# Optimization experiments

Measured on AMD Instinct MI355X. Metric: run time of the kernel, lower is better.

## Reference

```python
import jax, jax.numpy as jnp
import numpy as np

B, T = 4, 8
H, W = 120, 160
NON_SEM = 4
CAT = 16
MAP_CH = NON_SEM + CAT          # 20 map channels
FEAT_CH = 2 * NON_SEM + CAT     # 24 feature channels
RES = 5.0                       # cm per map cell
GLOBAL_M, LOCAL_M = 960, 240    # map_size/resolution, and /downscale
M2 = LOCAL_M * LOCAL_M
HFOV = 79.0
CAM_H_CM = 88.0
VISION_CM = 100 * RES           # vision_range cells -> cm
AGENT_R2 = 2.0 ** 2
EXPLORE_R2 = 3.0 ** 2
FX = W / (2.0 * float(np.tan(np.deg2rad(HFOV) / 2.0)))
FY = FX
CX, CY = W / 2.0, H / 2.0

LOCAL_POSE0 = jnp.array([LOCAL_M * RES / 2, LOCAL_M * RES / 2, 0.0], jnp.float32)
GLOBAL_POSE0 = jnp.array([GLOBAL_M * RES / 2, GLOBAL_M * RES / 2, 0.0], jnp.float32)
OFF = (GLOBAL_M - LOCAL_M) // 2
BOUNDS0 = jnp.array([OFF, OFF + LOCAL_M, OFF, OFF + LOCAL_M], jnp.int32)
ORIGINS0 = jnp.array([OFF * RES, OFF * RES, 0.0], jnp.float32)


def _splat1(flat, w):  # scatter-add scalar weights into the flattened local grid
    return jnp.zeros((M2,), jnp.float32).at[flat].add(w)


def _splatC(flat, vals):  # vals [C, N] -> [C, M2]
    return jnp.zeros((vals.shape[0], M2), jnp.float32).at[:, flat].add(vals)


def _step(carry, xs):
    lmap, gmap, lpose, gpose, bounds, origins = carry
    obs, delta, cam_T, done, upd = xs
    doneb = done != 0
    # per-env reset on episode end (init_map_and_pose_for_env)
    lmap = jnp.where(doneb[:, None, None, None], 0.0, lmap)
    gmap = jnp.where(doneb[:, None, None, None], 0.0, gmap)
    lpose = jnp.where(doneb[:, None], LOCAL_POSE0, lpose)
    gpose = jnp.where(doneb[:, None], GLOBAL_POSE0, gpose)
    bounds = jnp.where(doneb[:, None], BOUNDS0, bounds)
    origins = jnp.where(doneb[:, None], ORIGINS0, origins)

    # dead-reckoning pose update (delta in agent frame)
    th = jnp.deg2rad(lpose[:, 2])
    dx = delta[:, 0] * jnp.cos(th) - delta[:, 1] * jnp.sin(th)
    dy = delta[:, 0] * jnp.sin(th) + delta[:, 1] * jnp.cos(th)
    lpose = lpose + jnp.stack([dx, dy, delta[:, 2]], -1)

    # depth -> camera-frame point cloud (cm)
    depth = obs[:, 3] * 400.0 + 50.0  # [B,H,W]
    sem = obs[:, NON_SEM:]            # [B,CAT,H,W]
    uu = (jnp.arange(W, dtype=jnp.float32) - CX)[None, None, :]
    vv = (CY - jnp.arange(H, dtype=jnp.float32))[None, :, None]
    pts = jnp.stack([uu * depth / FX, vv * depth / FY, depth, jnp.ones_like(depth)], -1)
    pts = jnp.einsum('bij,bhwj->bhwi', cam_T, pts)  # camera extrinsics
    x_f, y_l, z_u = pts[..., 2], -pts[..., 0], pts[..., 1] + CAM_H_CM

    # agent frame -> local map frame
    th2 = jnp.deg2rad(lpose[:, 2])[:, None, None]
    wx = lpose[:, 0][:, None, None] + x_f * jnp.cos(th2) - y_l * jnp.sin(th2)
    wy = lpose[:, 1][:, None, None] + x_f * jnp.sin(th2) + y_l * jnp.cos(th2)
    ix = jnp.floor(wx / RES).astype(jnp.int32)
    iy = jnp.floor(wy / RES).astype(jnp.int32)
    valid = (depth > 25.0) & (depth < VISION_CM) & (ix >= 0) & (ix < LOCAL_M) & (iy >= 0) & (iy < LOCAL_M)
    flat = (jnp.clip(iy, 0, LOCAL_M - 1) * LOCAL_M + jnp.clip(ix, 0, LOCAL_M - 1)).reshape(B, -1)
    vm = valid.reshape(B, -1).astype(jnp.float32)
    obst_w = vm * ((z_u > 25.0) & (z_u < 150.0)).reshape(B, -1).astype(jnp.float32)

    exp_grid = jax.vmap(_splat1)(flat, vm).reshape(B, LOCAL_M, LOCAL_M)
    obst_grid = jax.vmap(_splat1)(flat, obst_w).reshape(B, LOCAL_M, LOCAL_M)
    sem_grid = jax.vmap(_splatC)(flat, sem.reshape(B, CAT, -1) * vm[:, None, :]).reshape(B, CAT, LOCAL_M, LOCAL_M)

    # agent location / been-close disks
    g = jnp.arange(LOCAL_M, dtype=jnp.float32)
    dxg = g[None, None, :] - (lpose[:, 0] / RES)[:, None, None]
    dyg = g[None, :, None] - (lpose[:, 1] / RES)[:, None, None]
    d2 = dxg * dxg + dyg * dyg
    agent = (d2 <= AGENT_R2).astype(jnp.float32)
    close = (d2 <= EXPLORE_R2).astype(jnp.float32)

    lmap = jnp.concatenate([
        jnp.maximum(lmap[:, 0], jnp.clip(obst_grid, 0.0, 1.0))[:, None],
        jnp.maximum(lmap[:, 1], jnp.clip(exp_grid, 0.0, 1.0))[:, None],
        agent[:, None],
        jnp.maximum(lmap[:, 3], close)[:, None],
        jnp.maximum(lmap[:, NON_SEM:], jnp.clip(sem_grid, 0.0, 1.0)),
    ], axis=1)

    # fuse local window into global map for envs flagged for update
    y1, x1 = bounds[:, 0], bounds[:, 2]
    crop = jax.vmap(lambda gm, y, x: jax.lax.dynamic_slice(gm, (0, y, x), (MAP_CH, LOCAL_M, LOCAL_M)))(gmap, y1, x1)
    updb = (upd != 0)[:, None, None, None]
    fused = jnp.where(updb, jnp.maximum(crop, lmap), crop)
    gmap = jax.vmap(lambda gm, c, y, x: jax.lax.dynamic_update_slice(gm, c, (0, y, x)))(gmap, fused, y1, x1)
    gpose = jnp.where((upd != 0)[:, None], lpose + origins, gpose)

    feats = jnp.concatenate([lmap[:, :NON_SEM], fused[:, :NON_SEM], lmap[:, NON_SEM:]], axis=1)
    return (lmap, gmap, lpose, gpose, bounds, origins), (feats, lpose, gpose, bounds, origins)


def _forward(obs_seq, pose_delta, cam_poses, init_local_map, init_global_map,
             init_local_pose, init_global_pose, init_origins,
             done_flags, update_flags, init_bounds):
    xs = (obs_seq.swapaxes(0, 1), pose_delta.swapaxes(0, 1), cam_poses.swapaxes(0, 1),
          done_flags.swapaxes(0, 1), update_flags.swapaxes(0, 1))
    carry0 = (init_local_map, init_global_map, init_local_pose, init_global_pose, init_bounds, init_origins)
    carry, ys = jax.lax.scan(_step, carry0, xs)
    feats, lp, gp, bnds, orgs = ys
    return (feats.swapaxes(0, 1), carry[0], carry[1], lp.swapaxes(0, 1), gp.swapaxes(0, 1),
            bnds.swapaxes(0, 1), orgs.swapaxes(0, 1))


def setup_inputs() -> dict:
    key = jax.random.key(0)
    ks = jax.random.split(key, 5)
    obs_seq = jax.random.uniform(ks[0], (B, T, MAP_CH, H, W), jnp.float32)
    pose_delta = jax.random.normal(ks[1], (B, T, 3), jnp.float32) * jnp.array([10.0, 2.0, 5.0], jnp.float32)
    cam_poses = jnp.eye(4, dtype=jnp.float32)[None, None] + 0.02 * jax.random.normal(ks[2], (B, T, 4, 4), jnp.float32)
    done_flags = jax.random.randint(ks[3], (B, T), 0, 2, jnp.int32)
    update_flags = jax.random.randint(ks[4], (B, T), 0, 2, jnp.int32)
    return {
        'obs_seq': obs_seq,
        'pose_delta': pose_delta,
        'done_flags': done_flags,
        'update_flags': update_flags,
        'cam_poses': cam_poses,
        'init_local_map': jnp.zeros((B, MAP_CH, LOCAL_M, LOCAL_M), jnp.float32),
        'init_global_map': jnp.zeros((B, MAP_CH, GLOBAL_M, GLOBAL_M), jnp.float32),
        'init_local_pose': jnp.tile(LOCAL_POSE0[None], (B, 1)),
        'init_global_pose': jnp.tile(GLOBAL_POSE0[None], (B, 1)),
        'init_bounds': jnp.tile(BOUNDS0[None], (B, 1)),
        'init_origins': jnp.tile(ORIGINS0[None], (B, 1)),
    }


def reference(obs_seq, pose_delta, done_flags, update_flags, cam_poses,
              init_local_map, init_global_map, init_local_pose, init_global_pose,
              init_bounds, init_origins):
    return _forward(obs_seq, pose_delta, cam_poses, init_local_map, init_global_map,
                    init_local_pose, init_global_pose, init_origins,
                    done_flags, update_flags, init_bounds)
```

## Files before the change

kernel.cpp:

```cpp
#include <hip/hip_runtime.h>
#include <math.h>

#define Bn 4
#define Tn 8
#define Hn 120
#define Wn 160
#define HWn (Hn * Wn)
#define NON_SEMn 4
#define CATn 16
#define MAP_CHn 20
#define FEAT_CHn 24
#define LOCAL_Mn 240
#define GLOBAL_Mn 960
#define M2n (LOCAL_Mn * LOCAL_Mn)
#define TBMn (Tn * Bn * M2n)
#define Pn (Tn * Bn * HWn)
#define NBLK_SCAN 1800
#define UPD_BLKS ((Bn * M2n + 255) / 256)
#define GMAP_BLKS ((Bn * MAP_CHn * GLOBAL_Mn * GLOBAL_Mn / 4 + 255) / 256)

#define DEG2RADf ((float)0.017453292519943295)

typedef float vf4 __attribute__((ext_vector_type(4)));

#define OUT_FEATS 0
#define OUT_LMAP  44236800
#define OUT_GMAP  48844800
#define OUT_LP    122572800
#define OUT_GP    122572896
#define OUT_BNDS  122572992
#define OUT_ORGS  122573120

#define WS_LPOSE  0
#define WS_ANYD   96
#define WS_REC2   128
#define WS_BSUM   (WS_REC2 + 2 * TBMn)
#define WS_CELL   (WS_BSUM + 2048)
#define WS_RECB   (WS_CELL + Pn)


__global__ void pose_kernel(const float* __restrict__ pose_delta,
                            const int* __restrict__ done_flags,
                            const int* __restrict__ upd_flags,
                            const float* __restrict__ init_lpose,
                            const float* __restrict__ init_gpose,
                            const int* __restrict__ init_bounds,
                            const float* __restrict__ init_origins,
                            float* __restrict__ ws_lpose,
                            float* __restrict__ ws_anydone,
                            float* __restrict__ out_lp,
                            float* __restrict__ out_gp,
                            float* __restrict__ out_bnds,
                            float* __restrict__ out_orgs) {
#pragma clang fp contract(off)
    int b = threadIdx.x;
    if (b >= Bn) return;
    float lx = init_lpose[b * 3 + 0], ly = init_lpose[b * 3 + 1], lz = init_lpose[b * 3 + 2];
    float gx = init_gpose[b * 3 + 0], gy = init_gpose[b * 3 + 1], gz = init_gpose[b * 3 + 2];
    int b0 = init_bounds[b * 4 + 0], b1 = init_bounds[b * 4 + 1];
    int b2i = init_bounds[b * 4 + 2], b3 = init_bounds[b * 4 + 3];
    float ox = init_origins[b * 3 + 0], oy = init_origins[b * 3 + 1], oz = init_origins[b * 3 + 2];
    float anyd = 0.0f;
    for (int t = 0; t < Tn; t++) {
        int done = done_flags[b * Tn + t];
        int upd  = upd_flags[b * Tn + t];
        if (done) {
            lx = 600.0f; ly = 600.0f; lz = 0.0f;
            gx = 2400.0f; gy = 2400.0f; gz = 0.0f;
            b0 = 360; b1 = 600; b2i = 360; b3 = 600;
            ox = 1800.0f; oy = 1800.0f; oz = 0.0f;
            anyd = 1.0f;
        }
        float th = lz * DEG2RADf;
        float c = cosf(th), s = sinf(th);
        float d0 = pose_delta[(b * Tn + t) * 3 + 0];
        float d1 = pose_delta[(b * Tn + t) * 3 + 1];
        float d2 = pose_delta[(b * Tn + t) * 3 + 2];
        lx = lx + (d0 * c - d1 * s);
        ly = ly + (d0 * s + d1 * c);
        lz = lz + d2;
        if (upd) { gx = lx + ox; gy = ly + oy; gz = lz + oz; }
        ws_lpose[(t * Bn + b) * 3 + 0] = lx;
        ws_lpose[(t * Bn + b) * 3 + 1] = ly;
        ws_lpose[(t * Bn + b) * 3 + 2] = lz;
        out_lp[(b * Tn + t) * 3 + 0] = lx;
        out_lp[(b * Tn + t) * 3 + 1] = ly;
        out_lp[(b * Tn + t) * 3 + 2] = lz;
        out_gp[(b * Tn + t) * 3 + 0] = gx;
        out_gp[(b * Tn + t) * 3 + 1] = gy;
        out_gp[(b * Tn + t) * 3 + 2] = gz;
        out_bnds[(b * Tn + t) * 4 + 0] = (float)b0;
        out_bnds[(b * Tn + t) * 4 + 1] = (float)b1;
        out_bnds[(b * Tn + t) * 4 + 2] = (float)b2i;
        out_bnds[(b * Tn + t) * 4 + 3] = (float)b3;
        out_orgs[(b * Tn + t) * 3 + 0] = ox;
        out_orgs[(b * Tn + t) * 3 + 1] = oy;
        out_orgs[(b * Tn + t) * 3 + 2] = oz;
    }
    ws_anydone[b] = anyd;
}

__global__ void project_kernel(const float* __restrict__ obs,
                               const float* __restrict__ cam,
                               const float* __restrict__ ws_lpose,
                               uint2* __restrict__ rec2,
                               int* __restrict__ cellid,
                               float fx) {
#pragma clang fp contract(off)
    int g = blockIdx.x * blockDim.x + threadIdx.x;
    if (g >= Pn) return;
    int p = g % HWn;
    int tb = g / HWn;
    int b = tb % Bn;
    int t = tb / Bn;
    int h = p / Wn, w = p % Wn;
    const float* ob = obs + (size_t)((b * Tn + t) * MAP_CHn) * HWn;
    float depth = ob[3 * HWn + p] * 400.0f + 50.0f;
    float u = (float)w - 80.0f;
    float v = 60.0f - (float)h;
    float px = u * depth / fx;
    float py = v * depth / fx;
    float pz = depth;
    const float* Tm = cam + (size_t)(b * Tn + t) * 16;
    float X = ((Tm[0] * px + Tm[1] * py) + Tm[2] * pz) + Tm[3];
    float Y = ((Tm[4] * px + Tm[5] * py) + Tm[6] * pz) + Tm[7];
    float Z = ((Tm[8] * px + Tm[9] * py) + Tm[10] * pz) + Tm[11];
    float x_f = Z;
    float y_l = -X;
    float z_u = Y + 88.0f;
    float lx = ws_lpose[(t * Bn + b) * 3 + 0];
    float ly = ws_lpose[(t * Bn + b) * 3 + 1];
    float lz = ws_lpose[(t * Bn + b) * 3 + 2];
    float th2 = lz * DEG2RADf;
    float c2 = cosf(th2), s2 = sinf(th2);
    float wx = (lx + x_f * c2) - y_l * s2;
    float wy = (ly + x_f * s2) + y_l * c2;
    int ix = (int)floorf(wx / 5.0f);
    int iy = (int)floorf(wy / 5.0f);
    bool valid = (depth > 25.0f) && (depth < 500.0f) &&
                 (ix >= 0) && (ix < LOCAL_Mn) && (iy >= 0) && (iy < LOCAL_Mn);
    int cell = -1;
    if (valid) {
        cell = (t * Bn + b) * M2n + iy * LOCAL_Mn + ix;
        unsigned addv = 1u + ((z_u > 25.0f && z_u < 150.0f) ? 65536u : 0u);
        atomicAdd(&rec2[cell].x, addv);
    }
    cellid[g] = cell;
}

__global__ void scan1_kernel(uint2* __restrict__ rec2,
                             unsigned* __restrict__ bsum) {
    __shared__ unsigned s[256];
    int tid = threadIdx.x;
    int base = blockIdx.x * 1024 + tid * 4;
    unsigned v0 = rec2[base].x & 0xFFFFu, v1 = rec2[base + 1].x & 0xFFFFu;
    unsigned v2 = rec2[base + 2].x & 0xFFFFu, v3 = rec2[base + 3].x & 0xFFFFu;
    unsigned tsum = v0 + v1 + v2 + v3;
    s[tid] = tsum;
    __syncthreads();
    for (int d = 1; d < 256; d <<= 1) {
        unsigned a = (tid >= d) ? s[tid - d] : 0u;
        __syncthreads();
        s[tid] += a;
        __syncthreads();
    }
    unsigned excl = s[tid] - tsum;
    if (tid == 255) bsum[blockIdx.x] = s[255];
    rec2[base].y     = excl;
    rec2[base + 1].y = excl + v0;
    rec2[base + 2].y = excl + v0 + v1;
    rec2[base + 3].y = excl + v0 + v1 + v2;
}

__global__ void scan2_kernel(unsigned* __restrict__ bsum) {
    __shared__ unsigned s[256];
    int tid = threadIdx.x;
    unsigned run = 0;
    for (int base = 0; base < NBLK_SCAN; base += 256) {
        int i = base + tid;
        unsigned v = (i < NBLK_SCAN) ? bsum[i] : 0u;
        s[tid] = v;
        __syncthreads();
        for (int d = 1; d < 256; d <<= 1) {
            unsigned a = (tid >= d) ? s[tid - d] : 0u;
            __syncthreads();
            s[tid] += a;
            __syncthreads();
        }
        unsigned tot = s[255];
        if (i < NBLK_SCAN) bsum[i] = run + s[tid] - v;
        run += tot;
        __syncthreads();
    }
}

__global__ void scatter_copy_kernel(const float* __restrict__ obs,
                                    const int* __restrict__ cellid,
                                    const unsigned* __restrict__ bsum,
                                    uint2* __restrict__ rec2,
                                    float* __restrict__ recb) {
    int g = blockIdx.x * blockDim.x + threadIdx.x;
    if (g >= Pn) return;
    int c = cellid[g];
    if (c < 0) return;
    int p = g % HWn;
    int tb = g / HWn;
    int b = tb % Bn;
    int t = tb / Bn;
    const float* ob = obs + (size_t)((b * Tn + t) * MAP_CHn) * HWn;
    vf4 r[4];
#pragma unroll
    for (int q = 0; q < 4; q++) {
        r[q].x = ob[(size_t)(NON_SEMn + 4 * q + 0) * HWn + p];
        r[q].y = ob[(size_t)(NON_SEMn + 4 * q + 1) * HWn + p];
        r[q].z = ob[(size_t)(NON_SEMn + 4 * q + 2) * HWn + p];
        r[q].w = ob[(size_t)(NON_SEMn + 4 * q + 3) * HWn + p];
    }
    unsigned pos = bsum[c >> 10] + atomicAdd(&rec2[c].y, 1u);
    vf4* rp = (vf4*)(recb + (size_t)pos * CATn);
#pragma unroll
    for (int q = 0; q < 4; q++)
        __builtin_nontemporal_store(r[q], rp + q);
}

__global__ void __launch_bounds__(256)
mega_kernel(const uint2* __restrict__ rec2,
            const unsigned* __restrict__ bsum,
            const float* __restrict__ recb,
            const int* __restrict__ done_flags,
            const int* __restrict__ upd_flags,
            const float* __restrict__ ws_lpose,
            const float* __restrict__ init_lmap,
            const float* __restrict__ init_gmap,
            const int* __restrict__ init_bounds,
            const float* __restrict__ anydone,
            float* __restrict__ out_feats,
            float* __restrict__ out_lmap,
            float* __restrict__ out_gmap) {
#pragma clang fp contract(off)
    if (blockIdx.x >= UPD_BLKS) {
        size_t i4 = (size_t)(blockIdx.x - UPD_BLKS) * blockDim.x + threadIdx.x;
        const size_t total4 = (size_t)Bn * MAP_CHn * GLOBAL_Mn * GLOBAL_Mn / 4;
        if (i4 >= total4) return;
        size_t f = i4 * 4;
        int gx = (int)(f % GLOBAL_Mn);
        size_t r = f / GLOBAL_Mn;
        int gy = (int)(r % GLOBAL_Mn);
        size_t bc = r / GLOBAL_Mn;
        int b = (int)(bc / MAP_CHn);
        int y1 = init_bounds[b * 4 + 0];
        int x1 = init_bounds[b * 4 + 2];
        if (gy >= y1 && gy < y1 + LOCAL_Mn && gx >= x1 && gx < x1 + LOCAL_Mn) return;
        vf4 v;
        if (anydone[b] != 0.0f) {
            v = (vf4)(0.0f);
        } else {
            v = __builtin_nontemporal_load((const vf4*)(init_gmap + f));
        }
        __builtin_nontemporal_store(v, (vf4*)(out_gmap + f));
        return;
    }

    int idx = blockIdx.x * blockDim.x + threadIdx.x;
    if (idx >= Bn * M2n) return;
    int b = idx / M2n, j = idx % M2n;
    int y = j / LOCAL_Mn, x = j % LOCAL_Mn;
    int y1 = init_bounds[b * 4 + 0];
    int x1 = init_bounds[b * 4 + 2];

    float lm[MAP_CHn], cr[MAP_CHn];
#pragma unroll
    for (int ch = 0; ch < MAP_CHn; ch++)
        lm[ch] = __builtin_nontemporal_load(init_lmap + ((size_t)(b * MAP_CHn + ch)) * M2n + j);
#pragma unroll
    for (int ch = 0; ch < MAP_CHn; ch++)
        cr[ch] = __builtin_nontemporal_load(
            init_gmap + ((size_t)(b * MAP_CHn + ch) * GLOBAL_Mn + (y1 + y)) * GLOBAL_Mn + (x1 + x));

    for (int t = 0; t < Tn; t++) {
        int done = done_flags[b * Tn + t];
        int upd  = upd_flags[b * Tn + t];
        if (done) {
#pragma unroll
            for (int ch = 0; ch < MAP_CHn; ch++) { lm[ch] = 0.0f; cr[ch] = 0.0f; }
        }
        float lx = ws_lpose[(t * Bn + b) * 3 + 0];
        float ly = ws_lpose[(t * Bn + b) * 3 + 1];
        float dxg = (float)x - lx / 5.0f;
        float dyg = (float)y - ly / 5.0f;
        float d2 = dxg * dxg + dyg * dyg;
        float agent = (d2 <= 4.0f) ? 1.0f : 0.0f;
        float close = (d2 <= 9.0f) ? 1.0f : 0.0f;

        int cell = (t * Bn + b) * M2n + j;
        uint2 rc = rec2[cell];
        unsigned n = rc.x & 0xFFFFu;
        lm[0] = fmaxf(lm[0], (rc.x >> 16) ? 1.0f : 0.0f);
        lm[1] = fmaxf(lm[1], n ? 1.0f : 0.0f);
        lm[2] = agent;
        lm[3] = fmaxf(lm[3], close);

        if (n) {
            unsigned st = bsum[cell >> 10] + rc.y - n;
            float sem[CATn];
#pragma unroll
            for (int c = 0; c < CATn; c++) sem[c] = 0.0f;
            const vf4* rp = (const vf4*)(recb + (size_t)st * CATn);
            for (unsigned k = 0; k < n; k++) {
                vf4 r0 = rp[0], r1 = rp[1], r2 = rp[2], r3 = rp[3];
                rp += 4;
                sem[0] += r0.x;  sem[1] += r0.y;  sem[2] += r0.z;  sem[3] += r0.w;
                sem[4] += r1.x;  sem[5] += r1.y;  sem[6] += r1.z;  sem[7] += r1.w;
                sem[8] += r2.x;  sem[9] += r2.y;  sem[10] += r2.z; sem[11] += r2.w;
                sem[12] += r3.x; sem[13] += r3.y; sem[14] += r3.z; sem[15] += r3.w;
            }
#pragma unroll
            for (int c = 0; c < CATn; c++)
                lm[NON_SEMn + c] = fmaxf(lm[NON_SEMn + c], fminf(fmaxf(sem[c], 0.0f), 1.0f));
        }
        if (upd) {
#pragma unroll
            for (int ch = 0; ch < MAP_CHn; ch++) cr[ch] = fmaxf(cr[ch], lm[ch]);
        }

        size_t fb = ((size_t)(b * Tn + t) * FEAT_CHn) * M2n + j;
#pragma unroll
        for (int ch = 0; ch < NON_SEMn; ch++)
            __builtin_nontemporal_store(lm[ch], out_feats + fb + (size_t)ch * M2n);
#pragma unroll
        for (int ch = 0; ch < NON_SEMn; ch++)
            __builtin_nontemporal_store(cr[ch], out_feats + fb + (size_t)(NON_SEMn + ch) * M2n);
#pragma unroll
        for (int c = 0; c < CATn; c++)
            __builtin_nontemporal_store(lm[NON_SEMn + c], out_feats + fb + (size_t)(2 * NON_SEMn + c) * M2n);
    }

#pragma unroll
    for (int ch = 0; ch < MAP_CHn; ch++)
        __builtin_nontemporal_store(lm[ch], out_lmap + ((size_t)(b * MAP_CHn + ch)) * M2n + j);
#pragma unroll
    for (int ch = 0; ch < MAP_CHn; ch++)
        __builtin_nontemporal_store(
            cr[ch], out_gmap + ((size_t)(b * MAP_CHn + ch) * GLOBAL_Mn + (y1 + y)) * GLOBAL_Mn + (x1 + x));
}

extern "C" void kernel_launch(void* const* d_in, const int* in_sizes, int n_in,
                              void* d_out, int out_size, void* d_ws, size_t ws_size,
                              hipStream_t stream) {
    const float* obs        = (const float*)d_in[0];
    const float* pose_delta = (const float*)d_in[1];
    const int*   done_flags = (const int*)d_in[2];
    const int*   upd_flags  = (const int*)d_in[3];
    const float* cam_poses  = (const float*)d_in[4];
    const float* init_lmap  = (const float*)d_in[5];
    const float* init_gmap  = (const float*)d_in[6];
    const float* init_lpose = (const float*)d_in[7];
    const float* init_gpose = (const float*)d_in[8];
    const int*   init_bnds  = (const int*)d_in[9];
    const float* init_orgs  = (const float*)d_in[10];

    float* out = (float*)d_out;
    float* ws  = (float*)d_ws;

    float*    ws_lpose = ws + WS_LPOSE;
    float*    ws_anyd  = ws + WS_ANYD;
    uint2*    rec2     = (uint2*)(ws + WS_REC2);
    unsigned* bsum     = (unsigned*)(ws + WS_BSUM);
    int*      cellid   = (int*)(ws + WS_CELL);
    float*    recb     = ws + WS_RECB;

    float fx = (float)(160.0 / (2.0 * tan(79.0 * M_PI / 180.0 / 2.0)));

    pose_kernel<<<1, 64, 0, stream>>>(pose_delta, done_flags, upd_flags,
                                      init_lpose, init_gpose, init_bnds, init_orgs,
                                      ws_lpose, ws_anyd,
                                      out + OUT_LP, out + OUT_GP,
                                      out + OUT_BNDS, out + OUT_ORGS);

    (void)hipMemsetAsync(rec2, 0, (size_t)TBMn * sizeof(uint2), stream);

    project_kernel<<<(Pn + 255) / 256, 256, 0, stream>>>(
        obs, cam_poses, ws_lpose, rec2, cellid, fx);

    scan1_kernel<<<NBLK_SCAN, 256, 0, stream>>>(rec2, bsum);
    scan2_kernel<<<1, 256, 0, stream>>>(bsum);

    scatter_copy_kernel<<<(Pn + 255) / 256, 256, 0, stream>>>(
        obs, cellid, bsum, rec2, recb);

    mega_kernel<<<UPD_BLKS + GMAP_BLKS, 256, 0, stream>>>(
        rec2, bsum, recb, done_flags, upd_flags, ws_lpose,
        init_lmap, init_gmap, init_bnds, ws_anyd,
        out + OUT_FEATS, out + OUT_LMAP, out + OUT_GMAP);
}
```

Measured before the change: 837.4 us.

## Fuse pose and global-map copy into projection; replace scan2 with atomic tile offsets

Drops the separate pose kernel: each projection and update thread recomputes its pose by replaying the dead-reckoning recurrence. The large global-map copy moves from the final update kernel into the projection launch, so that bandwidth-bound copy can overlap the atomic-heavy projection. The single-block scan2 kernel is replaced by an atomicAdd on a counter in scan1 that hands each tile a base offset. This works because tiles only need disjoint contiguous segments, not ordered ones. The change removes two launches and serial work at the cost of redundant per-thread trigonometry and unordered tile placement in the record buffer.

New measurement: 842.9 us. About the same (+0.7%).

```diff
diff --git a/kernel.cpp b/kernel.cpp
--- a/kernel.cpp
+++ b/kernel.cpp
@@ -15,8 +15,9 @@
 #define M2n (LOCAL_Mn * LOCAL_Mn)
 #define TBMn (Tn * Bn * M2n)
 #define Pn (Tn * Bn * HWn)
-#define NBLK_SCAN 1800
+#define NTILE_SCAN 1800
 #define UPD_BLKS ((Bn * M2n + 255) / 256)
+#define PROJ_BLKS ((Pn + 255) / 256)
 #define GMAP_BLKS ((Bn * MAP_CHn * GLOBAL_Mn * GLOBAL_Mn / 4 + 255) / 256)
 
 #define DEG2RADf ((float)0.017453292519943295)
@@ -31,46 +32,23 @@
 #define OUT_BNDS  122572992
 #define OUT_ORGS  122573120
 
-#define WS_LPOSE  0
-#define WS_ANYD   96
+#define WS_CNTR   96
 #define WS_REC2   128
 #define WS_BSUM   (WS_REC2 + 2 * TBMn)
 #define WS_CELL   (WS_BSUM + 2048)
 #define WS_RECB   (WS_CELL + Pn)
 
-
-__global__ void pose_kernel(const float* __restrict__ pose_delta,
-                            const int* __restrict__ done_flags,
-                            const int* __restrict__ upd_flags,
-                            const float* __restrict__ init_lpose,
-                            const float* __restrict__ init_gpose,
-                            const int* __restrict__ init_bounds,
-                            const float* __restrict__ init_origins,
-                            float* __restrict__ ws_lpose,
-                            float* __restrict__ ws_anydone,
-                            float* __restrict__ out_lp,
-                            float* __restrict__ out_gp,
-                            float* __restrict__ out_bnds,
-                            float* __restrict__ out_orgs) {
+__device__ __forceinline__ void pose_upto(const float* __restrict__ pose_delta,
+                                          const int* __restrict__ done_flags,
+                                          const float* __restrict__ init_lpose,
+                                          int b, int tt,
+                                          float& lx, float& ly, float& lz) {
 #pragma clang fp contract(off)
-    int b = threadIdx.x;
-    if (b >= Bn) return;
-    float lx = init_lpose[b * 3 + 0], ly = init_lpose[b * 3 + 1], lz = init_lpose[b * 3 + 2];
-    float gx = init_gpose[b * 3 + 0], gy = init_gpose[b * 3 + 1], gz = init_gpose[b * 3 + 2];
-    int b0 = init_bounds[b * 4 + 0], b1 = init_bounds[b * 4 + 1];
-    int b2i = init_bounds[b * 4 + 2], b3 = init_bounds[b * 4 + 3];
-    float ox = init_origins[b * 3 + 0], oy = init_origins[b * 3 + 1], oz = init_origins[b * 3 + 2];
-    float anyd = 0.0f;
-    for (int t = 0; t < Tn; t++) {
-        int done = done_flags[b * Tn + t];
-        int upd  = upd_flags[b * Tn + t];
-        if (done) {
-            lx = 600.0f; ly = 600.0f; lz = 0.0f;
-            gx = 2400.0f; gy = 2400.0f; gz = 0.0f;
-            b0 = 360; b1 = 600; b2i = 360; b3 = 600;
-            ox = 1800.0f; oy = 1800.0f; oz = 0.0f;
-            anyd = 1.0f;
-        }
+    lx = init_lpose[b * 3 + 0];
+    ly = init_lpose[b * 3 + 1];
+    lz = init_lpose[b * 3 + 2];
+    for (int t = 0; t <= tt; t++) {
+        if (done_flags[b * Tn + t]) { lx = 600.0f; ly = 600.0f; lz = 0.0f; }
         float th = lz * DEG2RADf;
         float c = cosf(th), s = sinf(th);
         float d0 = pose_delta[(b * Tn + t) * 3 + 0];
@@ -79,35 +57,96 @@
         lx = lx + (d0 * c - d1 * s);
         ly = ly + (d0 * s + d1 * c);
         lz = lz + d2;
-        if (upd) { gx = lx + ox; gy = ly + oy; gz = lz + oz; }
-        ws_lpose[(t * Bn + b) * 3 + 0] = lx;
-        ws_lpose[(t * Bn + b) * 3 + 1] = ly;
-        ws_lpose[(t * Bn + b) * 3 + 2] = lz;
-        out_lp[(b * Tn + t) * 3 + 0] = lx;
-        out_lp[(b * Tn + t) * 3 + 1] = ly;
-        out_lp[(b * Tn + t) * 3 + 2] = lz;
-        out_gp[(b * Tn + t) * 3 + 0] = gx;
-        out_gp[(b * Tn + t) * 3 + 1] = gy;
-        out_gp[(b * Tn + t) * 3 + 2] = gz;
-        out_bnds[(b * Tn + t) * 4 + 0] = (float)b0;
-        out_bnds[(b * Tn + t) * 4 + 1] = (float)b1;
-        out_bnds[(b * Tn + t) * 4 + 2] = (float)b2i;
-        out_bnds[(b * Tn + t) * 4 + 3] = (float)b3;
-        out_orgs[(b * Tn + t) * 3 + 0] = ox;
-        out_orgs[(b * Tn + t) * 3 + 1] = oy;
-        out_orgs[(b * Tn + t) * 3 + 2] = oz;
-    }
-    ws_anydone[b] = anyd;
-}
-
-__global__ void project_kernel(const float* __restrict__ obs,
-                               const float* __restrict__ cam,
-                               const float* __restrict__ ws_lpose,
-                               uint2* __restrict__ rec2,
-                               int* __restrict__ cellid,
-                               float fx) {
+    }
+}
+
+__global__ void __launch_bounds__(256)
+proj_gmap_kernel(const float* __restrict__ obs,
+                 const float* __restrict__ cam,
+                 const float* __restrict__ pose_delta,
+                 const int* __restrict__ done_flags,
+                 const int* __restrict__ upd_flags,
+                 const float* __restrict__ init_lpose,
+                 const float* __restrict__ init_gpose,
+                 const int* __restrict__ init_bounds,
+                 const float* __restrict__ init_origins,
+                 const float* __restrict__ init_gmap,
+                 uint2* __restrict__ rec2,
+                 int* __restrict__ cellid,
+                 float* __restrict__ out_lp,
+                 float* __restrict__ out_gp,
+                 float* __restrict__ out_bnds,
+                 float* __restrict__ out_orgs,
+                 float* __restrict__ out_gmap,
+                 float fx) {
 #pragma clang fp contract(off)
-    int g = blockIdx.x * blockDim.x + threadIdx.x;
+    if (blockIdx.x >= PROJ_BLKS) {
+        size_t i4 = (size_t)(blockIdx.x - PROJ_BLKS) * 256 + threadIdx.x;
+        const size_t total4 = (size_t)Bn * MAP_CHn * GLOBAL_Mn * GLOBAL_Mn / 4;
+        if (i4 >= total4) return;
+        size_t f = i4 * 4;
+        int gx = (int)(f % GLOBAL_Mn);
+        size_t r = f / GLOBAL_Mn;
+        int gy = (int)(r % GLOBAL_Mn);
+        size_t bc = r / GLOBAL_Mn;
+        int b = (int)(bc / MAP_CHn);
+        int y1 = init_bounds[b * 4 + 0];
+        int x1 = init_bounds[b * 4 + 2];
+        if (gy >= y1 && gy < y1 + LOCAL_Mn && gx >= x1 && gx < x1 + LOCAL_Mn) return;
+        bool anyd = false;
+        for (int t = 0; t < Tn; t++) anyd |= (done_flags[b * Tn + t] != 0);
+        vf4 v;
+        if (anyd) {
+            v = (vf4)(0.0f);
+        } else {
+            v = __builtin_nontemporal_load((const vf4*)(init_gmap + f));
+        }
+        __builtin_nontemporal_store(v, (vf4*)(out_gmap + f));
+        return;
+    }
+
+    if (blockIdx.x == 0 && threadIdx.x < Bn) {
+        int b = threadIdx.x;
+        float lx = init_lpose[b * 3 + 0], ly = init_lpose[b * 3 + 1], lz = init_lpose[b * 3 + 2];
+        float gx = init_gpose[b * 3 + 0], gy = init_gpose[b * 3 + 1], gz = init_gpose[b * 3 + 2];
+        int b0 = init_bounds[b * 4 + 0], b1 = init_bounds[b * 4 + 1];
+        int b2i = init_bounds[b * 4 + 2], b3 = init_bounds[b * 4 + 3];
+        float ox = init_origins[b * 3 + 0], oy = init_origins[b * 3 + 1], oz = init_origins[b * 3 + 2];
+        for (int t = 0; t < Tn; t++) {
+            int done = done_flags[b * Tn + t];
+            int upd  = upd_flags[b * Tn + t];
+            if (done) {
+                lx = 600.0f; ly = 600.0f; lz = 0.0f;
+                gx = 2400.0f; gy = 2400.0f; gz = 0.0f;
+                b0 = 360; b1 = 600; b2i = 360; b3 = 600;
+                ox = 1800.0f; oy = 1800.0f; oz = 0.0f;
+            }
+            float th = lz * DEG2RADf;
+            float c = cosf(th), sn = sinf(th);
+            float d0 = pose_delta[(b * Tn + t) * 3 + 0];
+            float d1 = pose_delta[(b * Tn + t) * 3 + 1];
+            float d2 = pose_delta[(b * Tn + t) * 3 + 2];
+            lx = lx + (d0 * c - d1 * sn);
+            ly = ly + (d0 * sn + d1 * c);
+            lz = lz + d2;
+            if (upd) { gx = lx + ox; gy = ly + oy; gz = lz + oz; }
+            out_lp[(b * Tn + t) * 3 + 0] = lx;
+            out_lp[(b * Tn + t) * 3 + 1] = ly;
+            out_lp[(b * Tn + t) * 3 + 2] = lz;
+            out_gp[(b * Tn + t) * 3 + 0] = gx;
+            out_gp[(b * Tn + t) * 3 + 1] = gy;
+            out_gp[(b * Tn + t) * 3 + 2] = gz;
+            out_bnds[(b * Tn + t) * 4 + 0] = (float)b0;
+            out_bnds[(b * Tn + t) * 4 + 1] = (float)b1;
+            out_bnds[(b * Tn + t) * 4 + 2] = (float)b2i;
+            out_bnds[(b * Tn + t) * 4 + 3] = (float)b3;
+            out_orgs[(b * Tn + t) * 3 + 0] = ox;
+            out_orgs[(b * Tn + t) * 3 + 1] = oy;
+            out_orgs[(b * Tn + t) * 3 + 2] = oz;
+        }
+    }
+
+    int g = blockIdx.x * 256 + threadIdx.x;
     if (g >= Pn) return;
     int p = g % HWn;
     int tb = g / HWn;
@@ -128,9 +167,8 @@
     float x_f = Z;
     float y_l = -X;
     float z_u = Y + 88.0f;
-    float lx = ws_lpose[(t * Bn + b) * 3 + 0];
-    float ly = ws_lpose[(t * Bn + b) * 3 + 1];
-    float lz = ws_lpose[(t * Bn + b) * 3 + 2];
+    float lx, ly, lz;
+    pose_upto(pose_delta, done_flags, init_lpose, b, t, lx, ly, lz);
     float th2 = lz * DEG2RADf;
     float c2 = cosf(th2), s2 = sinf(th2);
     float wx = (lx + x_f * c2) - y_l * s2;
@@ -149,7 +187,8 @@
 }
 
 __global__ void scan1_kernel(uint2* __restrict__ rec2,
-                             unsigned* __restrict__ bsum) {
+                             unsigned* __restrict__ bsum,
+                             unsigned* __restrict__ cntr) {
     __shared__ unsigned s[256];
     int tid = threadIdx.x;
     int base = blockIdx.x * 1024 + tid * 4;
@@ -165,33 +204,11 @@
         __syncthreads();
     }
     unsigned excl = s[tid] - tsum;
-    if (tid == 255) bsum[blockIdx.x] = s[255];
+    if (tid == 255) bsum[blockIdx.x] = atomicAdd(cntr, s[255]);
     rec2[base].y     = excl;
     rec2[base + 1].y = excl + v0;
     rec2[base + 2].y = excl + v0 + v1;
     rec2[base + 3].y = excl + v0 + v1 + v2;
-}
-
-__global__ void scan2_kernel(unsigned* __restrict__ bsum) {
-    __shared__ unsigned s[256];
-    int tid = threadIdx.x;
-    unsigned run = 0;
-    for (int base = 0; base < NBLK_SCAN; base += 256) {
-        int i = base + tid;
-        unsigned v = (i < NBLK_SCAN) ? bsum[i] : 0u;
-        s[tid] = v;
-        __syncthreads();
-        for (int d = 1; d < 256; d <<= 1) {
-            unsigned a = (tid >= d) ? s[tid - d] : 0u;
-            __syncthreads();
-            s[tid] += a;
-            __syncthreads();
-        }
-        unsigned tot = s[255];
-        if (i < NBLK_SCAN) bsum[i] = run + s[tid] - v;
-        run += tot;
-        __syncthreads();
-    }
 }
 
 __global__ void scatter_copy_kernel(const float* __restrict__ obs,
@@ -224,43 +241,20 @@
 }
 
 __global__ void __launch_bounds__(256)
-mega_kernel(const uint2* __restrict__ rec2,
-            const unsigned* __restrict__ bsum,
-            const float* __restrict__ recb,
-            const int* __restrict__ done_flags,
-            const int* __restrict__ upd_flags,
-            const float* __restrict__ ws_lpose,
-            const float* __restrict__ init_lmap,
-            const float* __restrict__ init_gmap,
-            const int* __restrict__ init_bounds,
-            const float* __restrict__ anydone,
-            float* __restrict__ out_feats,
-            float* __restrict__ out_lmap,
-            float* __restrict__ out_gmap) {
+update_kernel(const uint2* __restrict__ rec2,
+              const unsigned* __restrict__ bsum,
+              const float* __restrict__ recb,
+              const int* __restrict__ done_flags,
+              const int* __restrict__ upd_flags,
+              const float* __restrict__ pose_delta,
+              const float* __restrict__ init_lpose,
+              const float* __restrict__ init_lmap,
+              const float* __restrict__ init_gmap,
+              const int* __restrict__ init_bounds,
+              float* __restrict__ out_feats,
+              float* __restrict__ out_lmap,
+              float* __restrict__ out_gmap) {
 #pragma clang fp contract(off)
-    if (blockIdx.x >= UPD_BLKS) {
-        size_t i4 = (size_t)(blockIdx.x - UPD_BLKS) * blockDim.x + threadIdx.x;
-        const size_t total4 = (size_t)Bn * MAP_CHn * GLOBAL_Mn * GLOBAL_Mn / 4;
-        if (i4 >= total4) return;
-        size_t f = i4 * 4;
-        int gx = (int)(f % GLOBAL_Mn);
-        size_t r = f / GLOBAL_Mn;
-        int gy = (int)(r % GLOBAL_Mn);
-        size_t bc = r / GLOBAL_Mn;
-        int b = (int)(bc / MAP_CHn);
-        int y1 = init_bounds[b * 4 + 0];
-        int x1 = init_bounds[b * 4 + 2];
-        if (gy >= y1 && gy < y1 + LOCAL_Mn && gx >= x1 && gx < x1 + LOCAL_Mn) return;
-        vf4 v;
-        if (anydone[b] != 0.0f) {
-            v = (vf4)(0.0f);
-        } else {
-            v = __builtin_nontemporal_load((const vf4*)(init_gmap + f));
-        }
-        __builtin_nontemporal_store(v, (vf4*)(out_gmap + f));
-        return;
-    }
-
     int idx = blockIdx.x * blockDim.x + threadIdx.x;
     if (idx >= Bn * M2n) return;
     int b = idx / M2n, j = idx % M2n;
@@ -277,15 +271,28 @@
         cr[ch] = __builtin_nontemporal_load(
             init_gmap + ((size_t)(b * MAP_CHn + ch) * GLOBAL_Mn + (y1 + y)) * GLOBAL_Mn + (x1 + x));
 
+    float lx = init_lpose[b * 3 + 0];
+    float ly = init_lpose[b * 3 + 1];
+    float lz = init_lpose[b * 3 + 2];
+
     for (int t = 0; t < Tn; t++) {
         int done = done_flags[b * Tn + t];
         int upd  = upd_flags[b * Tn + t];
         if (done) {
 #pragma unroll
             for (int ch = 0; ch < MAP_CHn; ch++) { lm[ch] = 0.0f; cr[ch] = 0.0f; }
-        }
-        float lx = ws_lpose[(t * Bn + b) * 3 + 0];
-        float ly = ws_lpose[(t * Bn + b) * 3 + 1];
+            lx = 600.0f; ly = 600.0f; lz = 0.0f;
+        }
+        {
+            float th = lz * DEG2RADf;
+            float c = cosf(th), sn = sinf(th);
+            float d0 = pose_delta[(b * Tn + t) * 3 + 0];
+            float d1 = pose_delta[(b * Tn + t) * 3 + 1];
+            float d2p = pose_delta[(b * Tn + t) * 3 + 2];
+            lx = lx + (d0 * c - d1 * sn);
+            ly = ly + (d0 * sn + d1 * c);
+            lz = lz + d2p;
+        }
         float dxg = (float)x - lx / 5.0f;
         float dyg = (float)y - ly / 5.0f;
         float d2 = dxg * dxg + dyg * dyg;
@@ -362,34 +369,31 @@
     float* out = (float*)d_out;
     float* ws  = (float*)d_ws;
 
-    float*    ws_lpose = ws + WS_LPOSE;
-    float*    ws_anyd  = ws + WS_ANYD;
-    uint2*    rec2     = (uint2*)(ws + WS_REC2);
-    unsigned* bsum     = (unsigned*)(ws + WS_BSUM);
-    int*      cellid   = (int*)(ws + WS_CELL);
-    float*    recb     = ws + WS_RECB;
+    unsigned* cntr   = (unsigned*)(ws + WS_CNTR);
+    uint2*    rec2   = (uint2*)(ws + WS_REC2);
+    unsigned* bsum   = (unsigned*)(ws + WS_BSUM);
+    int*      cellid = (int*)(ws + WS_CELL);
+    float*    recb   = ws + WS_RECB;
 
     float fx = (float)(160.0 / (2.0 * tan(79.0 * M_PI / 180.0 / 2.0)));
 
-    pose_kernel<<<1, 64, 0, stream>>>(pose_delta, done_flags, upd_flags,
-                                      init_lpose, init_gpose, init_bnds, init_orgs,
-                                      ws_lpose, ws_anyd,
-                                      out + OUT_LP, out + OUT_GP,
-                                      out + OUT_BNDS, out + OUT_ORGS);
-
-    (void)hipMemsetAsync(rec2, 0, (size_t)TBMn * sizeof(uint2), stream);
-
-    project_kernel<<<(Pn + 255) / 256, 256, 0, stream>>>(
-        obs, cam_poses, ws_lpose, rec2, cellid, fx);
-
-    scan1_kernel<<<NBLK_SCAN, 256, 0, stream>>>(rec2, bsum);
-    scan2_kernel<<<1, 256, 0, stream>>>(bsum);
-
-    scatter_copy_kernel<<<(Pn + 255) / 256, 256, 0, stream>>>(
+    (void)hipMemsetAsync(ws + WS_CNTR, 0,
+                         (size_t)(32 + 2 * TBMn) * sizeof(float), stream);
+
+    proj_gmap_kernel<<<PROJ_BLKS + GMAP_BLKS, 256, 0, stream>>>(
+        obs, cam_poses, pose_delta, done_flags, upd_flags,
+        init_lpose, init_gpose, init_bnds, init_orgs, init_gmap,
+        rec2, cellid,
+        out + OUT_LP, out + OUT_GP, out + OUT_BNDS, out + OUT_ORGS,
+        out + OUT_GMAP, fx);
+
+    scan1_kernel<<<NTILE_SCAN, 256, 0, stream>>>(rec2, bsum, cntr);
+
+    scatter_copy_kernel<<<PROJ_BLKS, 256, 0, stream>>>(
         obs, cellid, bsum, rec2, recb);
 
-    mega_kernel<<<UPD_BLKS + GMAP_BLKS, 256, 0, stream>>>(
-        rec2, bsum, recb, done_flags, upd_flags, ws_lpose,
-        init_lmap, init_gmap, init_bnds, ws_anyd,
+    update_kernel<<<UPD_BLKS, 256, 0, stream>>>(
+        rec2, bsum, recb, done_flags, upd_flags, pose_delta, init_lpose,
+        init_lmap, init_gmap, init_bnds,
         out + OUT_FEATS, out + OUT_LMAP, out + OUT_GMAP);
 }
```
